# Kernel optimization log

Hardware: AMD Instinct MI355X
Metric: run time of the kernel (lower is better)

The kernel has to match this reference:

```python
import jax, jax.numpy as jnp
import numpy as np

K = 20
BN_EPS = 1e-5


def setup_inputs() -> dict:
    key = jax.random.key(0)
    ks = jax.random.split(key, 6)
    B, N, H = 2, 4096, 384
    s = lambda k, sh, sc: jax.random.normal(k, sh, dtype=jnp.float32) * sc
    return {
        "xyz": jax.random.normal(ks[0], (B, N, 3), dtype=jnp.float32),
        "W1": s(ks[1], (6, 128), 0.2),   "b1": jnp.zeros((128,), jnp.float32),
        "g1": jnp.ones((128,), jnp.float32), "be1": jnp.zeros((128,), jnp.float32),
        "W2": s(ks[2], (128, 256), 0.08), "b2": jnp.zeros((256,), jnp.float32),
        "W3": s(ks[3], (512, 512), 0.05), "b3": jnp.zeros((512,), jnp.float32),
        "g3": jnp.ones((512,), jnp.float32), "be3": jnp.zeros((512,), jnp.float32),
        "W4": s(ks[4], (512, H), 0.05),  "b4": jnp.zeros((H,), jnp.float32),
    }


def _knn_idx(x, k):
    # x: [B,N,3] -> k nearest neighbor indices (incl. self), sorted by distance
    sq = jnp.sum(x * x, axis=-1)                                  # [B,N]
    d2 = sq[:, :, None] + sq[:, None, :] - 2.0 * jnp.einsum('bnd,bmd->bnm', x, x)
    _, idx = jax.lax.top_k(-d2, k)                                # [B,N,k]
    return jax.lax.stop_gradient(idx)


def _bn_relu(h, gamma, beta):
    # BatchNorm1d in training mode: per-channel stats over (batch, length) dims.
    # h: [M, k, C]
    mu = jnp.mean(h, axis=(0, 1), keepdims=True)
    var = jnp.var(h, axis=(0, 1), keepdims=True)  # biased, matches torch BN
    return jax.nn.relu((h - mu) * jax.lax.rsqrt(var + BN_EPS) * gamma + beta)


def reference(xyz, W1, b1, g1, be1, W2, b2, W3, b3, g3, be3, W4, b4):
    B, N, _ = xyz.shape
    idx = _knn_idx(xyz, K)                                        # [B,N,K]
    nbr = jax.vmap(lambda pts, i: pts[i])(xyz, idx)               # [B,N,K,3]
    ctr = xyz[:, :, None, :]
    edge = jnp.concatenate([nbr - ctr, jnp.broadcast_to(ctr, nbr.shape)], axis=-1)
    h = edge.reshape(B * N, K, 6)                                 # [M,K,6]
    # conv1: Conv1d(6,128) -> BN -> ReLU -> Conv1d(128,256)  (kernel-1 convs == matmul)
    h = _bn_relu(h @ W1 + b1, g1, be1)
    h = h @ W2 + b2                                               # [M,K,256]
    gmax = jnp.max(h, axis=1, keepdims=True)                      # [M,1,256]
    f = jnp.concatenate([jnp.broadcast_to(gmax, h.shape), h], axis=-1)  # [M,K,512]
    # conv2: Conv1d(512,512) -> BN -> ReLU -> Conv1d(512,hidden)
    f = _bn_relu(f @ W3 + b3, g3, be3)
    f = f @ W4 + b4                                               # [M,K,H]
    feature = jnp.max(f, axis=1).reshape(B, N, -1)                # [B,N,H]
    return (xyz, feature)
```

## Files before the change

kernel.cpp:

```cpp
#include <hip/hip_runtime.h>
#include <float.h>

#define NPTS_B 4096
#define NPTS 8192
#define KNN 20
#define NSAMP (NPTS*KNN)

typedef __attribute__((ext_vector_type(8))) short bf16x8;
typedef __attribute__((ext_vector_type(4))) float f32x4;

static __device__ __forceinline__ float bf2f(unsigned short u) {
  return __uint_as_float(((unsigned int)u) << 16);
}
static __device__ __forceinline__ unsigned short f2bf(float f) {
  unsigned int u = __float_as_uint(f);
  u += 0x7fffu + ((u >> 16) & 1u);
  return (unsigned short)(u >> 16);
}
static __device__ __forceinline__ unsigned long long u64min(unsigned long long a,
                                                           unsigned long long b) {
  return a < b ? a : b;
}
static __device__ __forceinline__ unsigned long long shflx64(unsigned long long v, int m) {
  int lo = __shfl_xor((int)(unsigned int)(v & 0xffffffffull), m);
  int hi = __shfl_xor((int)(unsigned int)(v >> 32), m);
  return ((unsigned long long)(unsigned int)hi << 32) | (unsigned int)lo;
}
static __device__ __forceinline__ void gl_lds16(const void* g, void* l) {
  __builtin_amdgcn_global_load_lds(
      (const __attribute__((address_space(1))) unsigned int*)g,
      (__attribute__((address_space(3))) unsigned int*)l, 16, 0, 0);
}

__global__ __launch_bounds__(256) void wprep_kernel(const float* __restrict__ W3,
                                                    const float* __restrict__ W4,
                                                    const float* __restrict__ W2,
                                                    unsigned short* __restrict__ W3T,
                                                    unsigned short* __restrict__ W4T,
                                                    unsigned short* __restrict__ W2T) {
  int id = blockIdx.x * 256 + threadIdx.x;
  if (id < 512*512) {
    int n = id >> 9, k = id & 511;
    W3T[id] = f2bf(W3[k*512 + n]);
  } else if (id < 512*512 + 384*512) {
    int id2 = id - 512*512;
    int n = id2 >> 9, k = id2 & 511;
    W4T[id2] = f2bf(W4[k*384 + n]);
  } else {
    int id2 = id - (512*512 + 384*512);
    int n = id2 >> 7, k = id2 & 127;
    W2T[id2] = f2bf(W2[k*256 + n]);
  }
}

__global__ __launch_bounds__(256) void knn_kernel(const float* __restrict__ xyz,
                                                  int* __restrict__ idx,
                                                  float* __restrict__ out_xyz) {
#pragma clang fp contract(off)
  int p = blockIdx.x;
  int base = p & ~4095;
  int tid = threadIdx.x;
  int wv = tid >> 6;
  int ln = tid & 63;
  const float* xb = xyz + (size_t)base * 3;
  float xi0 = xyz[p*3+0], xi1 = xyz[p*3+1], xi2 = xyz[p*3+2];
  float sqi = (xi0*xi0 + xi1*xi1) + xi2*xi2;

  unsigned long long cand[16];
#pragma unroll
  for (int u = 0; u < 16; ++u) {
    int j = tid + (u << 8);
    float a0 = xb[j*3+0], a1 = xb[j*3+1], a2 = xb[j*3+2];
    float sqj = (a0*a0 + a1*a1) + a2*a2;
    float dt  = (xi0*a0 + xi1*a1) + xi2*a2;
    float d2  = (sqi + sqj) - 2.0f*dt;
    cand[u] = ((unsigned long long)__float_as_uint(d2) << 32) | (unsigned int)j;
  }
  unsigned long long myloc;
  {
    unsigned long long t[8];
#pragma unroll
    for (int u = 0; u < 8; ++u) t[u] = u64min(cand[u], cand[u + 8]);
#pragma unroll
    for (int u = 0; u < 4; ++u) t[u] = u64min(t[u], t[u + 4]);
    t[0] = u64min(t[0], t[2]); t[1] = u64min(t[1], t[3]);
    myloc = u64min(t[0], t[1]);
  }
  unsigned long long wmreg = myloc;
#pragma unroll
  for (int off = 1; off < 64; off <<= 1) wmreg = u64min(wmreg, shflx64(wmreg, off));

  __shared__ __align__(16) unsigned long long wbuf[2][4];
  __shared__ int outbuf[20];
  if (ln == 0) wbuf[0][wv] = wmreg;
  __syncthreads();

  for (int r = 0; r < 20; ++r) {
    int cur = r & 1;
    unsigned long long w0 = wbuf[cur][0], w1 = wbuf[cur][1];
    unsigned long long w2 = wbuf[cur][2], w3 = wbuf[cur][3];
    unsigned long long g = u64min(u64min(w0, w1), u64min(w2, w3));
    int wj = (int)(unsigned int)(g & 0xffffffffu);
    if (tid == (wj & 255)) {
      outbuf[r] = base + wj;
      unsigned long long m = ~0ull;
#pragma unroll
      for (int u = 0; u < 16; ++u) {
        if (cand[u] == g) cand[u] = ~0ull;
        m = u64min(m, cand[u]);
      }
      myloc = m;
    }
    if (wv == ((wj >> 6) & 3)) {
      unsigned long long t = myloc;
#pragma unroll
      for (int off = 1; off < 64; off <<= 1) t = u64min(t, shflx64(t, off));
      wmreg = t;
    }
    if (ln == 0) wbuf[cur ^ 1][wv] = wmreg;
    __syncthreads();
  }
  if (tid < 20) idx[p*20 + tid] = outbuf[tid];
  if (tid < 3) out_xyz[p*3 + tid] = xyz[p*3 + tid];
}

__global__ __launch_bounds__(256) void h1_moments_kernel(const float* __restrict__ xyz,
                                                         const int* __restrict__ idx,
                                                         float* __restrict__ mbuck) {
  int tid = threadIdx.x, blk = blockIdx.x;
  float A[33] = {};
#pragma unroll
  for (int u = 0; u < 2; ++u) {
    int s = blk*512 + (u << 8) + tid;
    unsigned int p = (unsigned int)s / 20u;
    int jg = idx[s];
    float c0 = xyz[p*3+0], c1 = xyz[p*3+1], c2 = xyz[p*3+2];
    float e[6];
    e[0] = xyz[jg*3+0] - c0; e[1] = xyz[jg*3+1] - c1; e[2] = xyz[jg*3+2] - c2;
    e[3] = c0; e[4] = c1; e[5] = c2;
    int k = 6;
#pragma unroll
    for (int d = 0; d < 6; ++d) {
      A[d] += e[d];
#pragma unroll
      for (int d2 = d; d2 < 6; ++d2) { A[k] = fmaf(e[d], e[d2], A[k]); ++k; }
    }
  }
#pragma unroll
  for (int off = 1; off < 64; off <<= 1) {
#pragma unroll
    for (int i = 0; i < 33; ++i) A[i] += __shfl_xor(A[i], off);
  }
  if ((tid & 63) == 0) {
    int b = ((blk << 2) | (tid >> 6)) & 15;
    for (int i = 0; i < 33; ++i) atomicAdd(&mbuck[b*64 + i], A[i]);
  }
}

__global__ void bn_prep1(const float* __restrict__ W1, const float* __restrict__ b1,
                         const float* __restrict__ g1, const float* __restrict__ be1,
                         const float* __restrict__ mbuck, float* __restrict__ misc) {
  __shared__ float red[33];
  int tid = threadIdx.x;
  if (tid < 33) {
    float s = 0.f;
    for (int b = 0; b < 16; ++b) s += mbuck[b*64 + tid];
    red[tid] = s;
  }
  __syncthreads();
  int c = tid;
  float w[6];
#pragma unroll
  for (int d = 0; d < 6; ++d) w[d] = W1[d*128 + c];
  const float inv = 1.0f / (float)NSAMP;
  float t = 0.f;
#pragma unroll
  for (int d = 0; d < 6; ++d) t = fmaf(w[d], red[d], t);
  t *= inv;
  float Q = 0.f;
  int k = 6;
#pragma unroll
  for (int d = 0; d < 6; ++d) {
#pragma unroll
    for (int d2 = d; d2 < 6; ++d2) {
      float coef = (d == d2) ? w[d]*w[d] : 2.f*w[d]*w[d2];
      Q = fmaf(coef, red[k], Q); ++k;
    }
  }
  Q *= inv;
  float var = Q - t*t;
  float mu = b1[c] + t;
  float a = g1[c] / sqrtf(var + 1e-5f);
  misc[c] = a;
  misc[128 + c] = be1[c] - mu*a;
}

__global__ __launch_bounds__(256) void h2_kernel(const float* __restrict__ xyz,
                                                 const int* __restrict__ idx,
                                                 const float* __restrict__ W1,
                                                 const float* __restrict__ b1,
                                                 const unsigned short* __restrict__ W2T,
                                                 const float* __restrict__ b2,
                                                 const float* __restrict__ misc,
                                                 unsigned short* __restrict__ h2out,
                                                 unsigned short* __restrict__ gmaxout) {
  int p0 = blockIdx.x << 2;
  int tid = threadIdx.x;
  int w = tid >> 6, lane = tid & 63;
  int lr = lane & 15, lg = lane >> 4;
  __shared__ float e[80][6];
  __shared__ __align__(16) unsigned short As[80][136];
  __shared__ float pool[20][264];

  bf16x8 bfr[4][4];
#pragma unroll
  for (int j = 0; j < 4; ++j)
#pragma unroll
    for (int kk = 0; kk < 4; ++kk)
      bfr[j][kk] = *(const bf16x8*)(W2T + (size_t)(w*64 + j*16 + lr)*128 + kk*32 + lg*8);

  if (tid < 80) {
    int pl = (unsigned int)tid / 20u;
    int p = p0 + pl;
    int jg = idx[p0*20 + tid];
    float xi0 = xyz[p*3+0], xi1 = xyz[p*3+1], xi2 = xyz[p*3+2];
    e[tid][0] = xyz[jg*3+0] - xi0;
    e[tid][1] = xyz[jg*3+1] - xi1;
    e[tid][2] = xyz[jg*3+2] - xi2;
    e[tid][3] = xi0; e[tid][4] = xi1; e[tid][5] = xi2;
  }
  __syncthreads();

  {
    int c = tid & 127, half = tid >> 7;
    float w1v[6];
#pragma unroll
    for (int d = 0; d < 6; ++d) w1v[d] = W1[d*128 + c];
    float b1v = b1[c], a1 = misc[c], d1 = misc[128 + c];
#pragma unroll
    for (int u = 0; u < 40; ++u) {
      int row = (u << 1) | half;
      float v = b1v;
#pragma unroll
      for (int d = 0; d < 6; ++d) v = fmaf(e[row][d], w1v[d], v);
      v = fmaxf(fmaf(a1, v, d1), 0.f);
      As[row][c] = f2bf(v);
    }
  }
  __syncthreads();

  f32x4 acc[5][4] = {};
#pragma unroll
  for (int kk = 0; kk < 4; ++kk) {
    bf16x8 a[5];
#pragma unroll
    for (int i = 0; i < 5; ++i)
      a[i] = *(const bf16x8*)&As[i*16 + lr][kk*32 + lg*8];
#pragma unroll
    for (int i = 0; i < 5; ++i)
#pragma unroll
      for (int j = 0; j < 4; ++j)
        acc[i][j] = __builtin_amdgcn_mfma_f32_16x16x32_bf16(a[i], bfr[j][kk], acc[i][j], 0, 0, 0);
  }

  float b2v[4];
#pragma unroll
  for (int j = 0; j < 4; ++j) b2v[j] = b2[w*64 + j*16 + lr];
#pragma unroll
  for (int i = 0; i < 5; ++i) {
    int rbase = p0*20 + i*16 + lg*4;
#pragma unroll
    for (int j = 0; j < 4; ++j) {
      int col = w*64 + j*16 + lr;
      float v0 = acc[i][j][0] + b2v[j];
      float v1 = acc[i][j][1] + b2v[j];
      float v2 = acc[i][j][2] + b2v[j];
      float v3 = acc[i][j][3] + b2v[j];
      h2out[(size_t)(rbase+0)*256 + col] = f2bf(v0);
      h2out[(size_t)(rbase+1)*256 + col] = f2bf(v1);
      h2out[(size_t)(rbase+2)*256 + col] = f2bf(v2);
      h2out[(size_t)(rbase+3)*256 + col] = f2bf(v3);
      pool[i*4 + lg][col] = fmaxf(fmaxf(v0, v1), fmaxf(v2, v3));
    }
  }
  __syncthreads();
#pragma unroll
  for (int l = 0; l < 4; ++l) {
    int id = tid + (l << 8);
    int q = id >> 8, col = id & 255;
    float v = pool[q*5][col];
#pragma unroll
    for (int u = 1; u < 5; ++u) v = fmaxf(v, pool[q*5 + u][col]);
    gmaxout[(size_t)(p0 + q)*256 + col] = f2bf(v);
  }
}

__global__ __launch_bounds__(256) void pgemm_kernel(const unsigned short* __restrict__ gmax,
                                                    const unsigned short* __restrict__ W3T,
                                                    unsigned short* __restrict__ Pg) {
  int bid = blockIdx.x;
  int bm = bid >> 1, bn = bid & 1;
  int m0 = bm << 6, n0 = bn << 8;
  int tid = threadIdx.x;
  int lane = tid & 63, w = tid >> 6;
  int lr = lane & 15, lg = lane >> 4;
  __shared__ __align__(16) char smem[40960];
  unsigned short (*As)[64] = (unsigned short (*)[64])smem;
  unsigned short (*Bs)[64] = (unsigned short (*)[64])(smem + 8192);
  unsigned short (*Cs)[264] = (unsigned short (*)[264])smem;

  int swz = lr >> 1;
  f32x4 acc[4][4] = {};
  for (int kc = 0; kc < 256; kc += 64) {
#pragma unroll
    for (int l = 0; l < 2; ++l) {
      int id = tid + (l << 8);
      int row = id >> 3, ks = id & 7, kg = ks ^ ((id >> 4) & 7);
      gl_lds16(gmax + (size_t)(m0 + row)*256 + kc + (kg << 3), &As[row][ks << 3]);
    }
#pragma unroll
    for (int l = 0; l < 8; ++l) {
      int id = tid + (l << 8);
      int row = id >> 3, ks = id & 7, kg = ks ^ ((id >> 4) & 7);
      gl_lds16(W3T + (size_t)(n0 + row)*512 + kc + (kg << 3), &Bs[row][ks << 3]);
    }
    __syncthreads();
#pragma unroll
    for (int h = 0; h < 2; ++h) {
      int ch = ((h << 2) | lg) ^ swz;
      bf16x8 a[4], b[4];
#pragma unroll
      for (int t = 0; t < 4; ++t)
        a[t] = *(const bf16x8*)&As[t*16 + lr][ch << 3];
#pragma unroll
      for (int t = 0; t < 4; ++t)
        b[t] = *(const bf16x8*)&Bs[w*64 + t*16 + lr][ch << 3];
#pragma unroll
      for (int i = 0; i < 4; ++i)
#pragma unroll
        for (int j = 0; j < 4; ++j)
          acc[i][j] = __builtin_amdgcn_mfma_f32_16x16x32_bf16(a[i], b[j], acc[i][j], 0, 0, 0);
    }
    __syncthreads();
  }
#pragma unroll
  for (int i = 0; i < 4; ++i)
#pragma unroll
    for (int j = 0; j < 4; ++j)
#pragma unroll
      for (int r = 0; r < 4; ++r)
        Cs[i*16 + lg*4 + r][w*64 + j*16 + lr] = f2bf(acc[i][j][r]);
  __syncthreads();
#pragma unroll
  for (int l = 0; l < 8; ++l) {
    int id = tid + (l << 8);
    int row = id >> 5, chk = id & 31;
    *(uint4*)(Pg + (size_t)(m0 + row)*512 + n0 + (chk << 3)) =
        *(const uint4*)&Cs[row][chk << 3];
  }
}

__global__ __launch_bounds__(512, 4) void gemm3_kernel(const unsigned short* __restrict__ h2,
                                                       const unsigned short* __restrict__ Pg,
                                                       const unsigned short* __restrict__ W3T,
                                                       const float* __restrict__ b3,
                                                       unsigned short* __restrict__ h3,
                                                       float* __restrict__ s3buck) {
  int bid = blockIdx.x;
  int grp = bid >> 4, rem = bid & 15;
  int bn = rem >> 3;
  int bm = (grp << 3) | (rem & 7);
  int m0 = bm << 7, n0 = bn << 8;
  int tid = threadIdx.x;
  int lane = tid & 63, w = tid >> 6;
  int mw = w >> 2, nw = w & 3;
  int lr = lane & 15, lg = lane >> 4;
  __shared__ __align__(16) char smem[51200];
  unsigned short (*As)[64] = (unsigned short (*)[64])smem;
  unsigned short (*Bs)[64] = (unsigned short (*)[64])(smem + 16384);
  float* ssum = (float*)(smem + 49152);
  float* ssq  = ssum + 256;
  unsigned short (*Cs)[264] = (unsigned short (*)[264])smem;

  int rS[4], ksS[4], kgS[4];
#pragma unroll
  for (int l = 0; l < 4; ++l) {
    int id = tid + (l << 9);
    rS[l] = id >> 3;
    ksS[l] = id & 7;
    kgS[l] = ksS[l] ^ ((id >> 4) & 7);
  }
  int swz = lr >> 1;

  f32x4 acc[4][4] = {};
  for (int kc = 0; kc < 256; kc += 64) {
#pragma unroll
    for (int l = 0; l < 2; ++l)
      gl_lds16(h2 + (size_t)(m0 + rS[l])*256 + kc + (kgS[l] << 3), &As[rS[l]][ksS[l] << 3]);
#pragma unroll
    for (int l = 0; l < 4; ++l)
      gl_lds16(W3T + (size_t)(n0 + rS[l])*512 + (kc + 256) + (kgS[l] << 3), &Bs[rS[l]][ksS[l] << 3]);
    __syncthreads();
#pragma unroll
    for (int h = 0; h < 2; ++h) {
      int ch = ((h << 2) | lg) ^ swz;
      bf16x8 a[4], b[4];
#pragma unroll
      for (int t = 0; t < 4; ++t)
        a[t] = *(const bf16x8*)&As[mw*64 + t*16 + lr][ch << 3];
#pragma unroll
      for (int t = 0; t < 4; ++t)
        b[t] = *(const bf16x8*)&Bs[nw*64 + t*16 + lr][ch << 3];
#pragma unroll
      for (int i = 0; i < 4; ++i)
#pragma unroll
        for (int j = 0; j < 4; ++j)
          acc[i][j] = __builtin_amdgcn_mfma_f32_16x16x32_bf16(a[i], b[j], acc[i][j], 0, 0, 0);
    }
    __syncthreads();
  }

  if (tid < 256) { ssum[tid] = 0.f; ssq[tid] = 0.f; }
  __syncthreads();
  unsigned int pt[4][4];
#pragma unroll
  for (int i = 0; i < 4; ++i) {
    int rbase = m0 + mw*64 + i*16 + lg*4;
#pragma unroll
    for (int r = 0; r < 4; ++r)
      pt[i][r] = (unsigned int)(rbase + r) / 20u;
  }
#pragma unroll
  for (int half = 0; half < 2; ++half) {
    if (mw == half) {
#pragma unroll
      for (int j = 0; j < 4; ++j) {
        int colL = nw*64 + j*16 + lr;
        float b3v = b3[n0 + colL];
        float sumv = 0.f, sqv = 0.f;
#pragma unroll
        for (int i = 0; i < 4; ++i) {
#pragma unroll
          for (int r = 0; r < 4; ++r) {
            float v = acc[i][j][r] + b3v +
                      bf2f(Pg[(size_t)pt[i][r]*512 + n0 + colL]);
            Cs[i*16 + lg*4 + r][colL] = f2bf(v);
            sumv += v; sqv = fmaf(v, v, sqv);
          }
        }
        sumv += __shfl_xor(sumv, 16); sumv += __shfl_xor(sumv, 32);
        sqv  += __shfl_xor(sqv, 16);  sqv  += __shfl_xor(sqv, 32);
        if (lg == 0) {
          atomicAdd(&ssum[colL], sumv);
          atomicAdd(&ssq[colL], sqv);
        }
      }
    }
    __syncthreads();
#pragma unroll
    for (int l = 0; l < 4; ++l) {
      int id = tid + (l << 9);
      int row = id >> 5, chk = id & 31;
      *(uint4*)(h3 + (size_t)(m0 + half*64 + row)*512 + n0 + (chk << 3)) =
          *(const uint4*)&Cs[row][chk << 3];
    }
    __syncthreads();
  }
  if (tid < 256) {
    int bkt = (bid & 63) * 1024;
    atomicAdd(&s3buck[bkt + n0 + tid], ssum[tid]);
    atomicAdd(&s3buck[bkt + 512 + n0 + tid], ssq[tid]);
  }
}

__global__ void bn_prep3(const float* __restrict__ g3, const float* __restrict__ be3,
                         const float* __restrict__ s3buck, float* __restrict__ misc) {
  int c = threadIdx.x;
  float s = 0.f, q = 0.f;
  for (int b = 0; b < 64; ++b) { s += s3buck[b*1024 + c]; q += s3buck[b*1024 + 512 + c]; }
  const float inv = 1.0f / (float)NSAMP;
  float mu = s * inv;
  float var = q * inv - mu * mu;
  float a = g3[c] / sqrtf(var + 1e-5f);
  misc[256 + c] = a;
  misc[768 + c] = be3[c] - mu * a;
}

__global__ __launch_bounds__(512) void gemm4_kernel(const unsigned short* __restrict__ h3,
                                                    const unsigned short* __restrict__ W4T,
                                                    const float* __restrict__ b4,
                                                    const float* __restrict__ misc,
                                                    float* __restrict__ outf) {
  int bm = blockIdx.x;
  int m0 = bm * 80;
  int tid = threadIdx.x;
  int lane = tid & 63, w = tid >> 6;
  int lr = lane & 15, lg = lane >> 4;
  __shared__ __align__(16) char smem[35072];
  unsigned short (*As)[40] = (unsigned short (*)[40])smem;
  unsigned short (*Bs)[32] = (unsigned short (*)[32])(smem + 6400);
  float (*pool)[392] = (float (*)[392])smem;
  float* af = (float*)(smem + 30976);
  float* df = af + 512;
  if (tid < 512) {
    af[tid] = misc[256 + tid];
    df[tid] = misc[768 + tid];
  }
  __syncthreads();
  f32x4 acc[5][3] = {};

  uint4 aR;
  int arow = tid >> 2, akg = tid & 3;
  if (tid < 320)
    aR = *(const uint4*)(h3 + (size_t)(m0 + arow)*512 + (akg << 3));
  int swz4 = (lr >> 1) & 3;

  for (int kc = 0; kc < 512; kc += 32) {
#pragma unroll
    for (int l = 0; l < 3; ++l) {
      int id = tid + (l << 9);
      int row = id >> 2, kgs = id & 3;
      int kg = kgs ^ ((row >> 1) & 3);
      gl_lds16(W4T + (size_t)row*512 + kc + (kg << 3), &Bs[row][kgs << 3]);
    }
    if (tid < 320) {
      int kb = kc + (akg << 3);
      unsigned int o[4];
#pragma unroll
      for (int q = 0; q < 4; ++q) {
        unsigned int u = ((const unsigned int*)&aR)[q];
        float lo = bf2f((unsigned short)(u & 0xffffu));
        float hi = bf2f((unsigned short)(u >> 16));
        int k0 = kb + q*2;
        lo = fmaxf(fmaf(af[k0],   lo, df[k0]),   0.f);
        hi = fmaxf(fmaf(af[k0+1], hi, df[k0+1]), 0.f);
        o[q] = (unsigned int)f2bf(lo) | ((unsigned int)f2bf(hi) << 16);
      }
      *(uint4*)&As[arow][akg << 3] = *(const uint4*)o;
    }
    __syncthreads();
    int kn = kc + 32;
    if (kn < 512 && tid < 320)
      aR = *(const uint4*)(h3 + (size_t)(m0 + arow)*512 + kn + (akg << 3));
    bf16x8 a[5], b[3];
#pragma unroll
    for (int t = 0; t < 5; ++t)
      a[t] = *(const bf16x8*)&As[t*16 + lr][lg << 3];
#pragma unroll
    for (int t = 0; t < 3; ++t)
      b[t] = *(const bf16x8*)&Bs[w*48 + t*16 + lr][(lg ^ swz4) << 3];
#pragma unroll
    for (int i = 0; i < 5; ++i)
#pragma unroll
      for (int j = 0; j < 3; ++j)
        acc[i][j] = __builtin_amdgcn_mfma_f32_16x16x32_bf16(a[i], b[j], acc[i][j], 0, 0, 0);
    __syncthreads();
  }

#pragma unroll
  for (int i = 0; i < 5; ++i)
#pragma unroll
    for (int j = 0; j < 3; ++j) {
      float m = fmaxf(fmaxf(acc[i][j][0], acc[i][j][1]),
                      fmaxf(acc[i][j][2], acc[i][j][3]));
      pool[i*4 + lg][w*48 + j*16 + lr] = m;
    }
  __syncthreads();
#pragma unroll
  for (int l = 0; l < 3; ++l) {
    int id = tid + (l << 9);
    int q = id / 384, c = id - q*384;
    float v = pool[q*5][c];
#pragma unroll
    for (int u = 1; u < 5; ++u) v = fmaxf(v, pool[q*5 + u][c]);
    outf[(size_t)(bm*4 + q)*384 + c] = v + b4[c];
  }
}

extern "C" void kernel_launch(void* const* d_in, const int* in_sizes, int n_in,
                              void* d_out, int out_size, void* d_ws, size_t ws_size,
                              hipStream_t stream) {
  const float* xyz = (const float*)d_in[0];
  const float* W1  = (const float*)d_in[1];
  const float* b1  = (const float*)d_in[2];
  const float* g1  = (const float*)d_in[3];
  const float* be1 = (const float*)d_in[4];
  const float* W2  = (const float*)d_in[5];
  const float* b2  = (const float*)d_in[6];
  const float* W3  = (const float*)d_in[7];
  const float* b3  = (const float*)d_in[8];
  const float* g3  = (const float*)d_in[9];
  const float* be3 = (const float*)d_in[10];
  const float* W4  = (const float*)d_in[11];
  const float* b4  = (const float*)d_in[12];

  char* ws = (char*)d_ws;
  int*            idx    = (int*)ws;
  float*          misc   = (float*)(ws + 0xA0000);
  float*          mbuck  = (float*)(ws + 0xA2000);
  float*          s3buck = (float*)(ws + 0xAA000);
  unsigned short* W3T    = (unsigned short*)(ws + 0xF0000);
  unsigned short* W4T    = (unsigned short*)(ws + 0x170000);
  unsigned short* W2T    = (unsigned short*)(ws + 0x1D0000);
  unsigned short* gmax   = (unsigned short*)(ws + 0x200000);
  unsigned short* h2     = (unsigned short*)(ws + 0x600000);
  unsigned short* h3     = (unsigned short*)(ws + 0x5600000ULL);
  unsigned short* Pg     = (unsigned short*)(ws + 0xF600000ULL);

  float* ofp   = (float*)d_out;
  float* oxyz  = ofp;
  float* ofeat = ofp + 24576;

  hipMemsetAsync(ws + 0xA2000, 0, 0x48000, stream);

  wprep_kernel<<<(512*512 + 384*512 + 256*128)/256, 256, 0, stream>>>(W3, W4, W2, W3T, W4T, W2T);
  knn_kernel<<<NPTS, 256, 0, stream>>>(xyz, idx, oxyz);
  h1_moments_kernel<<<NSAMP/512, 256, 0, stream>>>(xyz, idx, mbuck);
  bn_prep1<<<1, 128, 0, stream>>>(W1, b1, g1, be1, mbuck, misc);
  h2_kernel<<<NPTS/4, 256, 0, stream>>>(xyz, idx, W1, b1, W2T, b2, misc, h2, gmax);
  pgemm_kernel<<<256, 256, 0, stream>>>(gmax, W3T, Pg);
  gemm3_kernel<<<(NSAMP/128)*2, 512, 0, stream>>>(h2, Pg, W3T, b3, h3, s3buck);
  bn_prep3<<<1, 512, 0, stream>>>(g3, be3, s3buck, misc);
  gemm4_kernel<<<NPTS/4, 512, 0, stream>>>(h3, W4T, b4, misc, ofeat);
}
```

Before: 410.1 us.

## Replace iterative k-NN argmin rounds with histogram radix select and rank sort

Each k-NN block previously ran 20 rounds of block-wide argmin, with a wavefront shuffle reduction and a barrier in every round. The new kernel builds a 4096-bin shared-memory histogram on the top 12 bits of the distance keys and prefix-scans it to find the bin that holds the 20th neighbour. It then compacts the surviving candidates into shared memory and places each one by counting how many candidates are smaller. A small prep kernel also stores xyz as structure-of-arrays with precomputed squared norms, so the distance loads are coalesced. In exchange the kernel does shared-memory atomics, and the candidate list is capped at 2048 entries, which could drop neighbours if a bin is very crowded.

Result: faster. 351.6 us (-14.3%).

```diff
diff --git a/kernel.cpp b/kernel.cpp
--- a/kernel.cpp
+++ b/kernel.cpp
@@ -16,15 +16,6 @@
   unsigned int u = __float_as_uint(f);
   u += 0x7fffu + ((u >> 16) & 1u);
   return (unsigned short)(u >> 16);
-}
-static __device__ __forceinline__ unsigned long long u64min(unsigned long long a,
-                                                           unsigned long long b) {
-  return a < b ? a : b;
-}
-static __device__ __forceinline__ unsigned long long shflx64(unsigned long long v, int m) {
-  int lo = __shfl_xor((int)(unsigned int)(v & 0xffffffffull), m);
-  int hi = __shfl_xor((int)(unsigned int)(v >> 32), m);
-  return ((unsigned long long)(unsigned int)hi << 32) | (unsigned int)lo;
 }
 static __device__ __forceinline__ void gl_lds16(const void* g, void* l) {
   __builtin_amdgcn_global_load_lds(
@@ -53,74 +44,111 @@
   }
 }
 
+__global__ __launch_bounds__(256) void xyzprep_kernel(const float* __restrict__ xyz,
+                                                      float* __restrict__ xT) {
+#pragma clang fp contract(off)
+  int j = blockIdx.x * 256 + threadIdx.x;
+  int b = j >> 12, jj = j & 4095;
+  float x = xyz[j*3+0], y = xyz[j*3+1], z = xyz[j*3+2];
+  float sq = (x*x + y*y) + z*z;
+  float* base = xT + (size_t)b*16384;
+  base[jj] = x; base[4096+jj] = y; base[8192+jj] = z; base[12288+jj] = sq;
+}
+
 __global__ __launch_bounds__(256) void knn_kernel(const float* __restrict__ xyz,
+                                                  const float* __restrict__ xT,
                                                   int* __restrict__ idx,
                                                   float* __restrict__ out_xyz) {
 #pragma clang fp contract(off)
   int p = blockIdx.x;
-  int base = p & ~4095;
+  int b = p >> 12;
+  int base = b << 12;
   int tid = threadIdx.x;
-  int wv = tid >> 6;
-  int ln = tid & 63;
-  const float* xb = xyz + (size_t)base * 3;
+  const float* xb = xT + (size_t)b*16384;
   float xi0 = xyz[p*3+0], xi1 = xyz[p*3+1], xi2 = xyz[p*3+2];
   float sqi = (xi0*xi0 + xi1*xi1) + xi2*xi2;
 
+  __shared__ __align__(16) int hist[4096];
+  __shared__ int sL1[256];
+  __shared__ int nsel, binB;
+
+#pragma unroll
+  for (int u = 0; u < 16; ++u) hist[tid + (u << 8)] = 0;
+  if (tid == 0) nsel = 0;
+  __syncthreads();
+
   unsigned long long cand[16];
 #pragma unroll
   for (int u = 0; u < 16; ++u) {
     int j = tid + (u << 8);
-    float a0 = xb[j*3+0], a1 = xb[j*3+1], a2 = xb[j*3+2];
-    float sqj = (a0*a0 + a1*a1) + a2*a2;
+    float a0 = xb[j], a1 = xb[4096 + j], a2 = xb[8192 + j];
+    float sqj = xb[12288 + j];
     float dt  = (xi0*a0 + xi1*a1) + xi2*a2;
     float d2  = (sqi + sqj) - 2.0f*dt;
-    cand[u] = ((unsigned long long)__float_as_uint(d2) << 32) | (unsigned int)j;
-  }
-  unsigned long long myloc;
+    unsigned int kb = __float_as_uint(d2);
+    cand[u] = ((unsigned long long)kb << 32) | (unsigned int)j;
+    atomicAdd(&hist[kb >> 20], 1);
+  }
+  __syncthreads();
+
   {
-    unsigned long long t[8];
-#pragma unroll
-    for (int u = 0; u < 8; ++u) t[u] = u64min(cand[u], cand[u + 8]);
-#pragma unroll
-    for (int u = 0; u < 4; ++u) t[u] = u64min(t[u], t[u + 4]);
-    t[0] = u64min(t[0], t[2]); t[1] = u64min(t[1], t[3]);
-    myloc = u64min(t[0], t[1]);
-  }
-  unsigned long long wmreg = myloc;
-#pragma unroll
-  for (int off = 1; off < 64; off <<= 1) wmreg = u64min(wmreg, shflx64(wmreg, off));
-
-  __shared__ __align__(16) unsigned long long wbuf[2][4];
-  __shared__ int outbuf[20];
-  if (ln == 0) wbuf[0][wv] = wmreg;
-  __syncthreads();
-
-  for (int r = 0; r < 20; ++r) {
-    int cur = r & 1;
-    unsigned long long w0 = wbuf[cur][0], w1 = wbuf[cur][1];
-    unsigned long long w2 = wbuf[cur][2], w3 = wbuf[cur][3];
-    unsigned long long g = u64min(u64min(w0, w1), u64min(w2, w3));
-    int wj = (int)(unsigned int)(g & 0xffffffffu);
-    if (tid == (wj & 255)) {
-      outbuf[r] = base + wj;
-      unsigned long long m = ~0ull;
-#pragma unroll
-      for (int u = 0; u < 16; ++u) {
-        if (cand[u] == g) cand[u] = ~0ull;
-        m = u64min(m, cand[u]);
+    int s = 0;
+#pragma unroll
+    for (int u = 0; u < 16; ++u) s += hist[tid*16 + u];
+    sL1[tid] = s;
+  }
+  __syncthreads();
+
+  if (tid < 64) {
+    int v = sL1[tid*4] + sL1[tid*4+1] + sL1[tid*4+2] + sL1[tid*4+3];
+    int incl = v;
+#pragma unroll
+    for (int off = 1; off < 64; off <<= 1) {
+      int t = __shfl_up(incl, off);
+      if (tid >= off) incl += t;
+    }
+    unsigned long long ball = __ballot(incl >= KNN);
+    int L = __ffsll(ball) - 1;
+    if (tid == L) {
+      int cum = incl - v;
+      int bfound = -1;
+      for (int t2 = 4*L; t2 < 4*L + 4; ++t2) {
+        int s = sL1[t2];
+        if (bfound < 0) {
+          if (cum + s >= KNN) {
+            for (int u = 0; u < 16; ++u) {
+              int c = hist[t2*16 + u];
+              if (cum + c >= KNN) { bfound = t2*16 + u; break; }
+              cum += c;
+            }
+          } else {
+            cum += s;
+          }
+        }
       }
-      myloc = m;
-    }
-    if (wv == ((wj >> 6) & 3)) {
-      unsigned long long t = myloc;
-#pragma unroll
-      for (int off = 1; off < 64; off <<= 1) t = u64min(t, shflx64(t, off));
-      wmreg = t;
-    }
-    if (ln == 0) wbuf[cur ^ 1][wv] = wmreg;
-    __syncthreads();
-  }
-  if (tid < 20) idx[p*20 + tid] = outbuf[tid];
+      binB = bfound;
+    }
+  }
+  __syncthreads();
+
+  int B = binB;
+  unsigned long long* list = (unsigned long long*)hist;
+#pragma unroll
+  for (int u = 0; u < 16; ++u) {
+    if ((int)(unsigned int)(cand[u] >> 52) <= B) {
+      int pos = atomicAdd(&nsel, 1);
+      if (pos < 2048) list[pos] = cand[u];
+    }
+  }
+  __syncthreads();
+
+  int n = nsel; if (n > 2048) n = 2048;
+  for (int t = tid; t < n; t += 256) {
+    unsigned long long me = list[t];
+    int rank = 0;
+    for (int i = 0; i < n; ++i) rank += (list[i] < me);
+    if (rank < KNN) idx[p*20 + rank] = base + (int)(me & 0xffffffffu);
+  }
   if (tid < 3) out_xyz[p*3 + tid] = xyz[p*3 + tid];
 }
 
@@ -606,6 +634,7 @@
   unsigned short* h2     = (unsigned short*)(ws + 0x600000);
   unsigned short* h3     = (unsigned short*)(ws + 0x5600000ULL);
   unsigned short* Pg     = (unsigned short*)(ws + 0xF600000ULL);
+  float*          xT     = (float*)(ws + 0xFE00000ULL);
 
   float* ofp   = (float*)d_out;
   float* oxyz  = ofp;
@@ -614,7 +643,8 @@
   hipMemsetAsync(ws + 0xA2000, 0, 0x48000, stream);
 
   wprep_kernel<<<(512*512 + 384*512 + 256*128)/256, 256, 0, stream>>>(W3, W4, W2, W3T, W4T, W2T);
-  knn_kernel<<<NPTS, 256, 0, stream>>>(xyz, idx, oxyz);
+  xyzprep_kernel<<<NPTS/256, 256, 0, stream>>>(xyz, xT);
+  knn_kernel<<<NPTS, 256, 0, stream>>>(xyz, xT, idx, oxyz);
   h1_moments_kernel<<<NSAMP/512, 256, 0, stream>>>(xyz, idx, mbuck);
   bn_prep1<<<1, 128, 0, stream>>>(W1, b1, g1, be1, mbuck, misc);
   h2_kernel<<<NPTS/4, 256, 0, stream>>>(xyz, idx, W1, b1, W2T, b2, misc, h2, gmax);
```
